# Performance work log

Measured on AMD Instinct MI355X. Metric: run time of the kernel, lower is better.

The kernel has to match this reference:

```python
import jax, jax.numpy as jnp
import numpy as np

BN_EPS = 1e-5
W_EPS = 1e-8


def knn(query_xyz, key_xyz, k):
    # squared euclidean distances [B, Nq, Nk] via ||a||^2 + ||b||^2 - 2 a.b
    d = (jnp.sum(query_xyz ** 2, -1)[:, :, None]
         + jnp.sum(key_xyz ** 2, -1)[:, None, :]
         - 2.0 * jnp.einsum('bnd,bsd->bns', query_xyz, key_xyz))
    neg_d, idx = jax.lax.top_k(-d, k)  # k smallest distances
    return -neg_d, idx


def mlp_layer(x, w, b, g, beta):
    # Conv1d(kernel=1) == pointwise matmul; x: [B, N, Cin], w: [Cout, Cin]
    y = jnp.einsum('bnc,oc->bno', x, w) + b
    mean = jnp.mean(y, axis=(0, 1))          # BatchNorm1d training stats
    var = jnp.var(y, axis=(0, 1))            # biased variance (torch default)
    y = (y - mean) * jax.lax.rsqrt(var + BN_EPS) * g + beta
    return jax.nn.relu(y)


def setup_inputs() -> dict:
    key = jax.random.key(0)
    ks = jax.random.split(key, 12)
    B, S, N = 4, 4096, 16384
    Cs, Co = 256, 128
    Cin = Cs + Co
    C1, C2 = 256, 256
    return {
        'sampled_xyz': jax.random.normal(ks[0], (B, S, 3), jnp.float32),
        'sampled_features': jax.random.normal(ks[1], (B, S, Cs), jnp.float32),
        'original_xyz': jax.random.normal(ks[2], (B, N, 3), jnp.float32),
        'original_features': jax.random.normal(ks[3], (B, N, Co), jnp.float32),
        'w0': jax.random.normal(ks[4], (C1, Cin), jnp.float32) * (1.0 / np.sqrt(Cin)),
        'b0': jax.random.normal(ks[5], (C1,), jnp.float32) * 0.01,
        'g0': jnp.ones((C1,), jnp.float32),
        'bt0': jnp.zeros((C1,), jnp.float32),
        'w1': jax.random.normal(ks[6], (C2, C1), jnp.float32) * (1.0 / np.sqrt(C1)),
        'b1': jax.random.normal(ks[7], (C2,), jnp.float32) * 0.01,
        'g1': jnp.ones((C2,), jnp.float32),
        'bt1': jnp.zeros((C2,), jnp.float32),
        'k': 3,
    }


def reference(sampled_xyz, sampled_features, original_xyz, original_features,
              w0, b0, g0, bt0, w1, b1, g1, bt1, k):
    knn_dists, knn_idx = knn(original_xyz, sampled_xyz, k)      # [B, N, k]
    knn_w = 1.0 / (knn_dists + W_EPS)
    knn_w = knn_w / jnp.sum(knn_w, axis=-1, keepdims=True)
    # gather sampled features per neighbor: [B, N, k, Cs]
    knn_feats = jax.vmap(lambda f, i: f[i])(sampled_features, knn_idx)
    interp = jnp.sum(knn_feats * knn_w[:, :, :, None], axis=2)  # [B, N, Cs]
    x = jnp.concatenate([original_features, interp], axis=-1)    # [B, N, Co+Cs]
    x = mlp_layer(x, w0, b0, g0, bt0)
    x = mlp_layer(x, w1, b1, g1, bt1)
    return x
```

## Files before the change

kernel.cpp:

```cpp
#include <hip/hip_runtime.h>
#include <hip/hip_bf16.h>
#include <cstdint>
#include <cstddef>

#define Bn   4
#define Sn   4096
#define Nn   16384
#define CSn  256
#define COn  128
#define CINn 384
#define MTOT 65536

using short8 = short __attribute__((ext_vector_type(8)));
using f32x4  = float __attribute__((ext_vector_type(4)));
using f32x2  = float __attribute__((ext_vector_type(2)));

static __device__ __forceinline__ float bf2f(unsigned short u){
  unsigned int x = ((unsigned int)u) << 16;
  return __builtin_bit_cast(float, x);
}
static __device__ __forceinline__ unsigned short f2bf(float f){
  unsigned int x = __builtin_bit_cast(unsigned int, f);
  x += 0x7fffu + ((x >> 16) & 1u);
  return (unsigned short)(x >> 16);
}

static __device__ __forceinline__ void top3_insert(float d, int s,
    float& d0, float& d1, float& d2, int& i0, int& i1, int& i2){
  if (d < d2){
    if (d < d1){
      d2 = d1; i2 = i1;
      if (d < d0){ d1 = d0; i1 = i0; d0 = d; i0 = s; }
      else       { d1 = d;  i1 = s; }
    } else { d2 = d; i2 = s; }
  }
}

static __device__ __forceinline__ void top3_bf(float dd, int sidx,
    float& d0, float& d1, float& d2, int& i0, int& i1, int& i2){
  const bool c0 = dd < d0, c1 = dd < d1, c2 = dd < d2;
  const float od0 = d0, od1 = d1;
  d0 = fminf(dd, od0);
  d1 = __builtin_amdgcn_fmed3f(dd, od0, od1);
  d2 = __builtin_amdgcn_fmed3f(dd, od1, d2);
  i2 = c2 ? (c1 ? i1 : sidx) : i2;
  i1 = c1 ? (c0 ? i0 : sidx) : i1;
  i0 = c0 ? sidx : i0;
}

__global__ __launch_bounds__(256) void knn_kernel(
    const float* __restrict__ sxyz, const float* __restrict__ oxyz,
    float* __restrict__ kw, int* __restrict__ ki)
{
  __shared__ float4 cb[4][2][2][128];
  __shared__ float  md[4][64][3];
  __shared__ int    mi[4][64][3];

  const int b    = blockIdx.x >> 8;
  const int qblk = blockIdx.x & 255;
  const int lane = threadIdx.x & 63;
  const int wave = threadIdx.x >> 6;
  const int n    = qblk*64 + lane;
  const float* op = oxyz + ((size_t)b*Nn + n)*3;
  const float px = op[0], py = op[1], pz = op[2];
  const float qq = __fadd_rn(__fadd_rn(__fmul_rn(px,px), __fmul_rn(py,py)), __fmul_rn(pz,pz));
  const f32x2 px2 = {px,px}, py2 = {py,py}, pz2 = {pz,pz}, qq2 = {qq,qq};
  const f32x2 m2  = {-2.0f,-2.0f};

  const float* sx = sxyz + (size_t)b*Sn*3;
  const int qb = wave*1024;

  float ax[2], ay[2], az[2], bx[2], by[2], bz[2];

  #pragma unroll
  for (int it = 0; it < 2; ++it){
    int j  = it*64 + lane;
    int ja = qb + j, jb = ja + 512;
    ax[it]=sx[ja*3+0]; ay[it]=sx[ja*3+1]; az[it]=sx[ja*3+2];
    bx[it]=sx[jb*3+0]; by[it]=sx[jb*3+1]; bz[it]=sx[jb*3+2];
  }
  #pragma unroll
  for (int it = 0; it < 2; ++it){
    int j = it*64 + lane;
    float assv = __fadd_rn(__fadd_rn(__fmul_rn(ax[it],ax[it]), __fmul_rn(ay[it],ay[it])), __fmul_rn(az[it],az[it]));
    float bssv = __fadd_rn(__fadd_rn(__fmul_rn(bx[it],bx[it]), __fmul_rn(by[it],by[it])), __fmul_rn(bz[it],bz[it]));
    cb[wave][0][0][j] = make_float4(ax[it], bx[it], ay[it], by[it]);
    cb[wave][0][1][j] = make_float4(az[it], bz[it], assv, bssv);
  }

  float dA0=3.4e38f,dA1=3.4e38f,dA2=3.4e38f; int iA0=0,iA1=0,iA2=0;
  float dB0=3.4e38f,dB1=3.4e38f,dB2=3.4e38f; int iB0=0,iB1=0,iB2=0;

  int cur = 0;
  for (int c = 0; c < 4; ++c){
    if (c < 3){
      #pragma unroll
      for (int it = 0; it < 2; ++it){
        int j  = (c+1)*128 + it*64 + lane;
        int ja = qb + j, jb = ja + 512;
        ax[it]=sx[ja*3+0]; ay[it]=sx[ja*3+1]; az[it]=sx[ja*3+2];
        bx[it]=sx[jb*3+0]; by[it]=sx[jb*3+1]; bz[it]=sx[jb*3+2];
      }
    }
    const int base = qb + c*128;
    #pragma unroll 8
    for (int i = 0; i < 128; ++i){
      float4 lo = cb[wave][cur][0][i];
      float4 hi = cb[wave][cur][1][i];
      f32x2 kx2  = {lo.x, lo.y};
      f32x2 ky2  = {lo.z, lo.w};
      f32x2 kz2  = {hi.x, hi.y};
      f32x2 kss2 = {hi.z, hi.w};
      f32x2 dot = kx2 * px2;
      dot = __builtin_elementwise_fma(ky2, py2, dot);
      dot = __builtin_elementwise_fma(kz2, pz2, dot);
      f32x2 sm = qq2 + kss2;
      f32x2 dd = __builtin_elementwise_fma(m2, dot, sm);
      top3_bf(dd.x, base + i,       dA0,dA1,dA2, iA0,iA1,iA2);
      top3_bf(dd.y, base + i + 512, dB0,dB1,dB2, iB0,iB1,iB2);
    }
    if (c < 3){
      int nxt = cur ^ 1;
      #pragma unroll
      for (int it = 0; it < 2; ++it){
        int j = it*64 + lane;
        float assv = __fadd_rn(__fadd_rn(__fmul_rn(ax[it],ax[it]), __fmul_rn(ay[it],ay[it])), __fmul_rn(az[it],az[it]));
        float bssv = __fadd_rn(__fadd_rn(__fmul_rn(bx[it],bx[it]), __fmul_rn(by[it],by[it])), __fmul_rn(bz[it],bz[it]));
        cb[wave][nxt][0][j] = make_float4(ax[it], bx[it], ay[it], by[it]);
        cb[wave][nxt][1][j] = make_float4(az[it], bz[it], assv, bssv);
      }
      cur = nxt;
    }
  }

  {
    float e0=dA0, e1=dA1, e2=dA2; int j0=iA0, j1=iA1, j2=iA2;
    top3_insert(dB0, iB0, e0,e1,e2, j0,j1,j2);
    top3_insert(dB1, iB1, e0,e1,e2, j0,j1,j2);
    top3_insert(dB2, iB2, e0,e1,e2, j0,j1,j2);
    md[wave][lane][0]=e0; md[wave][lane][1]=e1; md[wave][lane][2]=e2;
    mi[wave][lane][0]=j0; mi[wave][lane][1]=j1; mi[wave][lane][2]=j2;
  }
  __syncthreads();
  if (threadIdx.x < 64){
    float e0=md[0][lane][0], e1=md[0][lane][1], e2=md[0][lane][2];
    int   j0=mi[0][lane][0], j1=mi[0][lane][1], j2=mi[0][lane][2];
    #pragma unroll
    for (int w = 1; w < 4; ++w){
      top3_insert(md[w][lane][0], mi[w][lane][0], e0,e1,e2, j0,j1,j2);
      top3_insert(md[w][lane][1], mi[w][lane][1], e0,e1,e2, j0,j1,j2);
      top3_insert(md[w][lane][2], mi[w][lane][2], e0,e1,e2, j0,j1,j2);
    }
    float wa = 1.0f/(e0+1e-8f), wb = 1.0f/(e1+1e-8f), wc = 1.0f/(e2+1e-8f);
    float sm = __fadd_rn(__fadd_rn(wa, wb), wc);
    size_t base = ((size_t)b*Nn + n)*3;
    kw[base+0] = wa/sm; kw[base+1] = wb/sm; kw[base+2] = wc/sm;
    ki[base+0] = j0;    ki[base+1] = j1;    ki[base+2] = j2;
  }
}

__global__ __launch_bounds__(256) void interp_kernel(
    const float* __restrict__ sfeat, const float* __restrict__ ofeat,
    const float* __restrict__ kw, const int* __restrict__ ki,
    unsigned short* __restrict__ X)
{
  const int c  = threadIdx.x;
  const int m0 = blockIdx.x * 16;
  for (int p = 0; p < 16; ++p){
    const int m = m0 + p;
    const int b = m >> 14;
    const float w0v = kw[(size_t)m*3+0], w1v = kw[(size_t)m*3+1], w2v = kw[(size_t)m*3+2];
    const int   i0  = ki[(size_t)m*3+0], i1  = ki[(size_t)m*3+1], i2  = ki[(size_t)m*3+2];
    const float* sb = sfeat + (size_t)b * Sn * CSn;
    float v = __fmaf_rn(w2v, sb[(size_t)i2*CSn + c],
              __fmaf_rn(w1v, sb[(size_t)i1*CSn + c],
              __fmul_rn(w0v, sb[(size_t)i0*CSn + c])));
    X[(size_t)m*CINn + COn + c] = f2bf(v);
    if (c < COn) X[(size_t)m*CINn + c] = f2bf(ofeat[(size_t)m*COn + c]);
  }
}

__global__ __launch_bounds__(256) void cvtw_kernel(
    const float* __restrict__ w0, const float* __restrict__ w1,
    unsigned short* __restrict__ w0b, unsigned short* __restrict__ w1b)
{
  int i = blockIdx.x*256 + threadIdx.x;
  if (i < 256*384) w0b[i] = f2bf(w0[i]);
  int j = i - 256*384;
  if (j >= 0 && j < 256*256) w1b[j] = f2bf(w1[j]);
}

template<int KDIM, bool BNRELU>
__global__ __launch_bounds__(256) void gemm_kernel(
    const unsigned short* __restrict__ A,
    const unsigned short* __restrict__ W,
    const float* __restrict__ bias,
    const float* __restrict__ s0sum,
    const float* __restrict__ s0sq,
    const float* __restrict__ bng,
    const float* __restrict__ bnbt,
    unsigned short* __restrict__ Y,
    float* __restrict__ osum,
    float* __restrict__ osq)
{
  __shared__ unsigned short As[128*64];
  __shared__ unsigned short Bs[256*64];
  __shared__ float lsc[256], lsh[256];
  const int tid  = threadIdx.x;
  const int lane = tid & 63;
  const int wave = tid >> 6;
  const size_t mbase = (size_t)blockIdx.x * 128;
  if constexpr (BNRELU){
    float mean = s0sum[tid] * (1.0f/65536.0f);
    float var  = s0sq[tid] * (1.0f/65536.0f) - mean*mean;
    float s = bng[tid] / sqrtf(var + 1e-5f);
    lsc[tid] = s;
    lsh[tid] = __fmaf_rn(-mean, s, bnbt[tid]);
  }
  f32x4 acc[8][4];
  #pragma unroll
  for (int m2 = 0; m2 < 8; ++m2)
    #pragma unroll
    for (int n2 = 0; n2 < 4; ++n2) acc[m2][n2] = f32x4{0.f,0.f,0.f,0.f};
  __syncthreads();

  for (int k0 = 0; k0 < KDIM; k0 += 64){
    if (k0) __syncthreads();
    #pragma unroll
    for (int i = 0; i < 4; ++i){
      int cid = tid + 256*i;
      int row = cid >> 3, c8 = cid & 7;
      short8 v = *reinterpret_cast<const short8*>(A + (mbase+row)*KDIM + k0 + c8*8);
      if constexpr (BNRELU){
        #pragma unroll
        for (int j = 0; j < 8; ++j){
          int kc = k0 + c8*8 + j;
          float f = bf2f((unsigned short)v[j]);
          f = fmaxf(__fmaf_rn(f, lsc[kc], lsh[kc]), 0.0f);
          v[j] = (short)f2bf(f);
        }
      }
      *reinterpret_cast<short8*>(reinterpret_cast<char*>(As) + row*128 + ((c8 ^ (row&7)) << 4)) = v;
    }
    #pragma unroll
    for (int i = 0; i < 8; ++i){
      int cid = tid + 256*i;
      int row = cid >> 3, c8 = cid & 7;
      short8 v = *reinterpret_cast<const short8*>(W + (size_t)row*KDIM + k0 + c8*8);
      *reinterpret_cast<short8*>(reinterpret_cast<char*>(Bs) + row*128 + ((c8 ^ (row&7)) << 4)) = v;
    }
    __syncthreads();
    #pragma unroll
    for (int kk = 0; kk < 2; ++kk){
      short8 af[8], bv[4];
      #pragma unroll
      for (int m2 = 0; m2 < 8; ++m2){
        int row = m2*16 + (lane & 15);
        int c8  = kk*4 + (lane >> 4);
        af[m2] = *reinterpret_cast<const short8*>(reinterpret_cast<char*>(As) + row*128 + ((c8 ^ (row&7)) << 4));
      }
      #pragma unroll
      for (int n2 = 0; n2 < 4; ++n2){
        int row = wave*64 + n2*16 + (lane & 15);
        int c8  = kk*4 + (lane >> 4);
        bv[n2] = *reinterpret_cast<const short8*>(reinterpret_cast<char*>(Bs) + row*128 + ((c8 ^ (row&7)) << 4));
      }
      #pragma unroll
      for (int m2 = 0; m2 < 8; ++m2)
        #pragma unroll
        for (int n2 = 0; n2 < 4; ++n2)
          acc[m2][n2] = __builtin_amdgcn_mfma_f32_16x16x32_bf16(af[m2], bv[n2], acc[m2][n2], 0, 0, 0);
    }
  }

  const int colg0 = wave*64;
  float spart[4] = {0,0,0,0}, qpart[4] = {0,0,0,0};
  #pragma unroll
  for (int m2 = 0; m2 < 8; ++m2){
    #pragma unroll
    for (int n2 = 0; n2 < 4; ++n2){
      const int gc  = colg0 + n2*16 + (lane & 15);
      const float bvv = bias[gc];
      #pragma unroll
      for (int j = 0; j < 4; ++j){
        float yv = acc[m2][n2][j] + bvv;
        size_t gr = mbase + m2*16 + (lane>>4)*4 + j;
        Y[gr*256 + gc] = f2bf(yv);
        spart[n2] += yv;
        qpart[n2] = __fmaf_rn(yv, yv, qpart[n2]);
      }
    }
  }
  #pragma unroll
  for (int n2 = 0; n2 < 4; ++n2){
    float s = spart[n2], q = qpart[n2];
    s += __shfl_xor(s, 16); q += __shfl_xor(q, 16);
    s += __shfl_xor(s, 32); q += __shfl_xor(q, 32);
    if (lane < 16){
      int gc = colg0 + n2*16 + lane;
      atomicAdd(&osum[gc], s);
      atomicAdd(&osq[gc], q);
    }
  }
}

__global__ __launch_bounds__(256) void apply_kernel(
    const unsigned short* __restrict__ y,
    const float* __restrict__ s1sum, const float* __restrict__ s1sq,
    const float* __restrict__ g, const float* __restrict__ bt,
    float* __restrict__ out)
{
  __shared__ float ssc[256], ssh[256];
  {
    int c = threadIdx.x;
    float mean = s1sum[c] * (1.0f/65536.0f);
    float var  = s1sq[c] * (1.0f/65536.0f) - mean*mean;
    float s = g[c] / sqrtf(var + 1e-5f);
    ssc[c] = s;
    ssh[c] = __fmaf_rn(-mean, s, bt[c]);
  }
  __syncthreads();
  const int t = blockIdx.x*256 + threadIdx.x;
  const size_t base = (size_t)t * 8;
  const int c0 = (int)(base & 255);
  short8 v = *reinterpret_cast<const short8*>(y + base);
  float r[8];
  #pragma unroll
  for (int j = 0; j < 8; ++j){
    float f = bf2f((unsigned short)v[j]);
    f = __fmaf_rn(f, ssc[c0+j], ssh[c0+j]);
    r[j] = fmaxf(f, 0.0f);
  }
  float4 o0, o1;
  o0.x=r[0]; o0.y=r[1]; o0.z=r[2]; o0.w=r[3];
  o1.x=r[4]; o1.y=r[5]; o1.z=r[6]; o1.w=r[7];
  *reinterpret_cast<float4*>(out + base)     = o0;
  *reinterpret_cast<float4*>(out + base + 4) = o1;
}

constexpr size_t WS_STATS = 0;
constexpr size_t WS_W0B   = 8192;
constexpr size_t WS_W1B   = WS_W0B + 196608;
constexpr size_t WS_KW    = WS_W1B + 131072;
constexpr size_t WS_KI    = WS_KW + 786432;
constexpr size_t WS_X     = 4194304;
constexpr size_t WS_Y0    = WS_X + (size_t)MTOT*CINn*2;

extern "C" void kernel_launch(void* const* d_in, const int* in_sizes, int n_in,
                              void* d_out, int out_size, void* d_ws, size_t ws_size,
                              hipStream_t stream)
{
  const float* sxyz  = (const float*)d_in[0];
  const float* sfeat = (const float*)d_in[1];
  const float* oxyz  = (const float*)d_in[2];
  const float* ofeat = (const float*)d_in[3];
  const float* w0    = (const float*)d_in[4];
  const float* b0    = (const float*)d_in[5];
  const float* g0    = (const float*)d_in[6];
  const float* bt0   = (const float*)d_in[7];
  const float* w1    = (const float*)d_in[8];
  const float* b1    = (const float*)d_in[9];
  const float* g1    = (const float*)d_in[10];
  const float* bt1   = (const float*)d_in[11];

  char* ws = (char*)d_ws;
  float* stats  = (float*)(ws + WS_STATS);
  unsigned short* w0b = (unsigned short*)(ws + WS_W0B);
  unsigned short* w1b = (unsigned short*)(ws + WS_W1B);
  float* kw = (float*)(ws + WS_KW);
  int*   ki = (int*)(ws + WS_KI);
  unsigned short* X  = (unsigned short*)(ws + WS_X);
  unsigned short* Y0 = (unsigned short*)(ws + WS_Y0);
  unsigned short* Y1 = (unsigned short*)(ws + WS_X);

  hipMemsetAsync(stats, 0, 4*256*sizeof(float), stream);
  cvtw_kernel<<<640, 256, 0, stream>>>(w0, w1, w0b, w1b);
  knn_kernel<<<1024, 256, 0, stream>>>(sxyz, oxyz, kw, ki);
  interp_kernel<<<MTOT/16, 256, 0, stream>>>(sfeat, ofeat, kw, ki, X);
  gemm_kernel<CINn, false><<<MTOT/128, 256, 0, stream>>>(
      X, w0b, b0, nullptr, nullptr, nullptr, nullptr, Y0, stats, stats + 256);
  gemm_kernel<256, true><<<MTOT/128, 256, 0, stream>>>(
      Y0, w1b, b1, stats, stats + 256, g0, bt0, Y1, stats + 512, stats + 768);
  apply_kernel<<<(MTOT*256)/(256*8), 256, 0, stream>>>(
      Y1, stats + 512, stats + 768, g1, bt1, (float*)d_out);
}
```

Measured before the change: 275.2 us.

## Split KNN key range across two blocks and merge partial top-3 in separate kernel

The KNN kernel now splits the 4096 sampled points into 8 slices across two blocks per query tile, doubling the grid to 2048 blocks. Each wave writes its partial top-3 distances and indices to workspace, and a new merge kernel combines the 8 partials and computes the normalized weights. This replaces the in-block shared-memory reduction and syncthreads with more parallelism and better occupancy. The cost is an extra kernel launch and global traffic for the partial results.

New measurement: 277.4 us. About the same (+0.8%).

```diff
diff --git a/kernel.cpp b/kernel.cpp
--- a/kernel.cpp
+++ b/kernel.cpp
@@ -50,42 +50,37 @@
 
 __global__ __launch_bounds__(256) void knn_kernel(
     const float* __restrict__ sxyz, const float* __restrict__ oxyz,
-    float* __restrict__ kw, int* __restrict__ ki)
-{
-  __shared__ float4 cb[4][2][2][128];
-  __shared__ float  md[4][64][3];
-  __shared__ int    mi[4][64][3];
-
-  const int b    = blockIdx.x >> 8;
-  const int qblk = blockIdx.x & 255;
+    float* __restrict__ PD, int* __restrict__ PI)
+{
+  __shared__ float4 cb[4][2][2][64];
+
+  const int b    = blockIdx.x >> 9;
+  const int qblk = (blockIdx.x >> 1) & 255;
+  const int half = blockIdx.x & 1;
   const int lane = threadIdx.x & 63;
   const int wave = threadIdx.x >> 6;
-  const int n    = qblk*64 + lane;
-  const float* op = oxyz + ((size_t)b*Nn + n)*3;
+  const int gq   = b*Nn + qblk*64 + lane;
+  const float* op = oxyz + (size_t)gq*3;
   const float px = op[0], py = op[1], pz = op[2];
   const float qq = __fadd_rn(__fadd_rn(__fmul_rn(px,px), __fmul_rn(py,py)), __fmul_rn(pz,pz));
   const f32x2 px2 = {px,px}, py2 = {py,py}, pz2 = {pz,pz}, qq2 = {qq,qq};
   const f32x2 m2  = {-2.0f,-2.0f};
 
   const float* sx = sxyz + (size_t)b*Sn*3;
-  const int qb = wave*1024;
-
-  float ax[2], ay[2], az[2], bx[2], by[2], bz[2];
-
-  #pragma unroll
-  for (int it = 0; it < 2; ++it){
-    int j  = it*64 + lane;
-    int ja = qb + j, jb = ja + 512;
-    ax[it]=sx[ja*3+0]; ay[it]=sx[ja*3+1]; az[it]=sx[ja*3+2];
-    bx[it]=sx[jb*3+0]; by[it]=sx[jb*3+1]; bz[it]=sx[jb*3+2];
-  }
-  #pragma unroll
-  for (int it = 0; it < 2; ++it){
-    int j = it*64 + lane;
-    float assv = __fadd_rn(__fadd_rn(__fmul_rn(ax[it],ax[it]), __fmul_rn(ay[it],ay[it])), __fmul_rn(az[it],az[it]));
-    float bssv = __fadd_rn(__fadd_rn(__fmul_rn(bx[it],bx[it]), __fmul_rn(by[it],by[it])), __fmul_rn(bz[it],bz[it]));
-    cb[wave][0][0][j] = make_float4(ax[it], bx[it], ay[it], by[it]);
-    cb[wave][0][1][j] = make_float4(az[it], bz[it], assv, bssv);
+  const int slice = half*4 + wave;
+  const int sbase = half*2048 + wave*512;
+
+  float ax, ay, az, bx, by, bz;
+  {
+    int ja = sbase + lane, jb = ja + 256;
+    ax=sx[ja*3+0]; ay=sx[ja*3+1]; az=sx[ja*3+2];
+    bx=sx[jb*3+0]; by=sx[jb*3+1]; bz=sx[jb*3+2];
+  }
+  {
+    float assv = __fadd_rn(__fadd_rn(__fmul_rn(ax,ax), __fmul_rn(ay,ay)), __fmul_rn(az,az));
+    float bssv = __fadd_rn(__fadd_rn(__fmul_rn(bx,bx), __fmul_rn(by,by)), __fmul_rn(bz,bz));
+    cb[wave][0][0][lane] = make_float4(ax, bx, ay, by);
+    cb[wave][0][1][lane] = make_float4(az, bz, assv, bssv);
   }
 
   float dA0=3.4e38f,dA1=3.4e38f,dA2=3.4e38f; int iA0=0,iA1=0,iA2=0;
@@ -94,17 +89,13 @@
   int cur = 0;
   for (int c = 0; c < 4; ++c){
     if (c < 3){
-      #pragma unroll
-      for (int it = 0; it < 2; ++it){
-        int j  = (c+1)*128 + it*64 + lane;
-        int ja = qb + j, jb = ja + 512;
-        ax[it]=sx[ja*3+0]; ay[it]=sx[ja*3+1]; az[it]=sx[ja*3+2];
-        bx[it]=sx[jb*3+0]; by[it]=sx[jb*3+1]; bz[it]=sx[jb*3+2];
-      }
-    }
-    const int base = qb + c*128;
+      int ja = sbase + (c+1)*64 + lane, jb = ja + 256;
+      ax=sx[ja*3+0]; ay=sx[ja*3+1]; az=sx[ja*3+2];
+      bx=sx[jb*3+0]; by=sx[jb*3+1]; bz=sx[jb*3+2];
+    }
+    const int base = sbase + c*64;
     #pragma unroll 8
-    for (int i = 0; i < 128; ++i){
+    for (int i = 0; i < 64; ++i){
       float4 lo = cb[wave][cur][0][i];
       float4 hi = cb[wave][cur][1][i];
       f32x2 kx2  = {lo.x, lo.y};
@@ -117,46 +108,50 @@
       f32x2 sm = qq2 + kss2;
       f32x2 dd = __builtin_elementwise_fma(m2, dot, sm);
       top3_bf(dd.x, base + i,       dA0,dA1,dA2, iA0,iA1,iA2);
-      top3_bf(dd.y, base + i + 512, dB0,dB1,dB2, iB0,iB1,iB2);
+      top3_bf(dd.y, base + i + 256, dB0,dB1,dB2, iB0,iB1,iB2);
     }
     if (c < 3){
       int nxt = cur ^ 1;
-      #pragma unroll
-      for (int it = 0; it < 2; ++it){
-        int j = it*64 + lane;
-        float assv = __fadd_rn(__fadd_rn(__fmul_rn(ax[it],ax[it]), __fmul_rn(ay[it],ay[it])), __fmul_rn(az[it],az[it]));
-        float bssv = __fadd_rn(__fadd_rn(__fmul_rn(bx[it],bx[it]), __fmul_rn(by[it],by[it])), __fmul_rn(bz[it],bz[it]));
-        cb[wave][nxt][0][j] = make_float4(ax[it], bx[it], ay[it], by[it]);
-        cb[wave][nxt][1][j] = make_float4(az[it], bz[it], assv, bssv);
-      }
+      float assv = __fadd_rn(__fadd_rn(__fmul_rn(ax,ax), __fmul_rn(ay,ay)), __fmul_rn(az,az));
+      float bssv = __fadd_rn(__fadd_rn(__fmul_rn(bx,bx), __fmul_rn(by,by)), __fmul_rn(bz,bz));
+      cb[wave][nxt][0][lane] = make_float4(ax, bx, ay, by);
+      cb[wave][nxt][1][lane] = make_float4(az, bz, assv, bssv);
       cur = nxt;
     }
   }
 
-  {
-    float e0=dA0, e1=dA1, e2=dA2; int j0=iA0, j1=iA1, j2=iA2;
-    top3_insert(dB0, iB0, e0,e1,e2, j0,j1,j2);
-    top3_insert(dB1, iB1, e0,e1,e2, j0,j1,j2);
-    top3_insert(dB2, iB2, e0,e1,e2, j0,j1,j2);
-    md[wave][lane][0]=e0; md[wave][lane][1]=e1; md[wave][lane][2]=e2;
-    mi[wave][lane][0]=j0; mi[wave][lane][1]=j1; mi[wave][lane][2]=j2;
-  }
-  __syncthreads();
-  if (threadIdx.x < 64){
-    float e0=md[0][lane][0], e1=md[0][lane][1], e2=md[0][lane][2];
-    int   j0=mi[0][lane][0], j1=mi[0][lane][1], j2=mi[0][lane][2];
-    #pragma unroll
-    for (int w = 1; w < 4; ++w){
-      top3_insert(md[w][lane][0], mi[w][lane][0], e0,e1,e2, j0,j1,j2);
-      top3_insert(md[w][lane][1], mi[w][lane][1], e0,e1,e2, j0,j1,j2);
-      top3_insert(md[w][lane][2], mi[w][lane][2], e0,e1,e2, j0,j1,j2);
-    }
-    float wa = 1.0f/(e0+1e-8f), wb = 1.0f/(e1+1e-8f), wc = 1.0f/(e2+1e-8f);
-    float sm = __fadd_rn(__fadd_rn(wa, wb), wc);
-    size_t base = ((size_t)b*Nn + n)*3;
-    kw[base+0] = wa/sm; kw[base+1] = wb/sm; kw[base+2] = wc/sm;
-    ki[base+0] = j0;    ki[base+1] = j1;    ki[base+2] = j2;
-  }
+  top3_insert(dB0, iB0, dA0,dA1,dA2, iA0,iA1,iA2);
+  top3_insert(dB1, iB1, dA0,dA1,dA2, iA0,iA1,iA2);
+  top3_insert(dB2, iB2, dA0,dA1,dA2, iA0,iA1,iA2);
+  PD[(slice*3+0)*MTOT + gq] = dA0;
+  PD[(slice*3+1)*MTOT + gq] = dA1;
+  PD[(slice*3+2)*MTOT + gq] = dA2;
+  PI[(slice*3+0)*MTOT + gq] = iA0;
+  PI[(slice*3+1)*MTOT + gq] = iA1;
+  PI[(slice*3+2)*MTOT + gq] = iA2;
+}
+
+__global__ __launch_bounds__(256) void knnmerge_kernel(
+    const float* __restrict__ PD, const int* __restrict__ PI,
+    float* __restrict__ kw, int* __restrict__ ki)
+{
+  const int gq = blockIdx.x*256 + threadIdx.x;
+  float e0=3.4e38f, e1=3.4e38f, e2=3.4e38f;
+  int   j0=0, j1=0, j2=0;
+  #pragma unroll
+  for (int s = 0; s < 8; ++s){
+    #pragma unroll
+    for (int j = 0; j < 3; ++j){
+      float d = PD[(s*3+j)*MTOT + gq];
+      int   i = PI[(s*3+j)*MTOT + gq];
+      top3_insert(d, i, e0,e1,e2, j0,j1,j2);
+    }
+  }
+  float wa = 1.0f/(e0+1e-8f), wb = 1.0f/(e1+1e-8f), wc = 1.0f/(e2+1e-8f);
+  float sm = __fadd_rn(__fadd_rn(wa, wb), wc);
+  size_t base = (size_t)gq*3;
+  kw[base+0] = wa/sm; kw[base+1] = wb/sm; kw[base+2] = wc/sm;
+  ki[base+0] = j0;    ki[base+1] = j1;    ki[base+2] = j2;
 }
 
 __global__ __launch_bounds__(256) void interp_kernel(
@@ -345,6 +340,8 @@
 constexpr size_t WS_KI    = WS_KW + 786432;
 constexpr size_t WS_X     = 4194304;
 constexpr size_t WS_Y0    = WS_X + (size_t)MTOT*CINn*2;
+constexpr size_t WS_PD    = WS_X;
+constexpr size_t WS_PI    = WS_X + (size_t)8*3*MTOT*4;
 
 extern "C" void kernel_launch(void* const* d_in, const int* in_sizes, int n_in,
                               void* d_out, int out_size, void* d_ws, size_t ws_size,
@@ -369,13 +366,16 @@
   unsigned short* w1b = (unsigned short*)(ws + WS_W1B);
   float* kw = (float*)(ws + WS_KW);
   int*   ki = (int*)(ws + WS_KI);
+  float* PD = (float*)(ws + WS_PD);
+  int*   PI = (int*)(ws + WS_PI);
   unsigned short* X  = (unsigned short*)(ws + WS_X);
   unsigned short* Y0 = (unsigned short*)(ws + WS_Y0);
   unsigned short* Y1 = (unsigned short*)(ws + WS_X);
 
   hipMemsetAsync(stats, 0, 4*256*sizeof(float), stream);
   cvtw_kernel<<<640, 256, 0, stream>>>(w0, w1, w0b, w1b);
-  knn_kernel<<<1024, 256, 0, stream>>>(sxyz, oxyz, kw, ki);
+  knn_kernel<<<2048, 256, 0, stream>>>(sxyz, oxyz, PD, PI);
+  knnmerge_kernel<<<MTOT/256, 256, 0, stream>>>(PD, PI, kw, ki);
   interp_kernel<<<MTOT/16, 256, 0, stream>>>(sfeat, ofeat, kw, ki, X);
   gemm_kernel<CINn, false><<<MTOT/128, 256, 0, stream>>>(
       X, w0b, b0, nullptr, nullptr, nullptr, nullptr, Y0, stats, stats + 256);
```
